# Performance work log

Hardware: AMD Instinct MI355X
Metric: run time of the kernel (lower is better)

Reference implementation:

```python
import jax, jax.numpy as jnp
import numpy as np

N, E, D_IN, HID, D_OUT, HEADS = 4096, 262144, 256, 256, 128, 4


def gcn_conv(x, edge_index, edge_weight, W, b):
    # PyG GCNConv: linear -> gcn_norm (add self loops, sym norm) -> scatter-add -> +bias
    n = x.shape[0]
    row, col = edge_index[0], edge_index[1]
    loop = jnp.arange(n)
    row_f = jnp.concatenate([row, loop])
    col_f = jnp.concatenate([col, loop])
    ew_f = jnp.concatenate([edge_weight, jnp.ones((n,), edge_weight.dtype)])
    deg = jax.ops.segment_sum(ew_f, col_f, num_segments=n)
    dinv = jnp.where(deg > 0, jax.lax.rsqrt(deg), 0.0)
    norm = dinv[row_f] * ew_f * dinv[col_f]  # [E+N]
    h = x @ W                                # [N, out]
    out = jax.ops.segment_sum(norm[:, None] * h[row_f], col_f, num_segments=n)
    return out + b


def mha(x, in_proj_w, in_proj_b, out_proj_w, out_proj_b):
    # torch.nn.MultiheadAttention, unbatched input [L, Emb], q=k=v=x
    L, Emb = x.shape
    dh = Emb // HEADS
    qkv = x @ in_proj_w.T + in_proj_b
    q, k, v = jnp.split(qkv, 3, axis=-1)
    rs = lambda t: t.reshape(L, HEADS, dh).transpose(1, 0, 2)  # [H, L, dh]
    q, k, v = rs(q), rs(k), rs(v)
    scores = jnp.einsum('hld,hmd->hlm', q, k) / np.float32(np.sqrt(dh))
    attn = jax.nn.softmax(scores, axis=-1)
    o = jnp.einsum('hlm,hmd->hld', attn, v).transpose(1, 0, 2).reshape(L, Emb)
    return o @ out_proj_w.T + out_proj_b


def setup_inputs() -> dict:
    key = jax.random.key(0)
    ks = jax.random.split(key, 12)
    s = 0.02
    return {
        'node_features': jax.random.normal(ks[0], (N, D_IN), jnp.float32),
        'edge_index': jax.random.randint(ks[1], (2, E), 0, N),
        'edge_weight': jax.random.uniform(ks[2], (E,), jnp.float32),
        'W1': jax.random.normal(ks[3], (D_IN, HID), jnp.float32) * s,
        'b1': jnp.zeros((HID,), jnp.float32),
        'W2': jax.random.normal(ks[4], (HID, HID), jnp.float32) * s,
        'b2': jnp.zeros((HID,), jnp.float32),
        'W3': jax.random.normal(ks[5], (HID, D_OUT), jnp.float32) * s,
        'b3': jnp.zeros((D_OUT,), jnp.float32),
        'in_proj_w': jax.random.normal(ks[6], (3 * HID, HID), jnp.float32) * s,
        'in_proj_b': jnp.zeros((3 * HID,), jnp.float32),
        'out_proj_w': jax.random.normal(ks[7], (HID, HID), jnp.float32) * s,
        'out_proj_b': jnp.zeros((HID,), jnp.float32),
    }


def reference(node_features, edge_index, edge_weight, W1, b1, W2, b2, W3, b3,
              in_proj_w, in_proj_b, out_proj_w, out_proj_b):
    ew = edge_weight.astype(jnp.float32)
    x = gcn_conv(node_features, edge_index, ew, W1, b1)
    x = jax.nn.relu(mha(x, in_proj_w, in_proj_b, out_proj_w, out_proj_b))
    # dropout is identity at inference
    x = gcn_conv(x, edge_index, ew, W2, b2)
    x = jax.nn.relu(mha(x, in_proj_w, in_proj_b, out_proj_w, out_proj_b))
    x = gcn_conv(x, edge_index, ew, W3, b3)
    return jax.nn.sigmoid(x)
```

## Files before the change

kernel.cpp:

```cpp
#include <hip/hip_runtime.h>
#include <math.h>

#define N_NODES 4096
#define N_EDGES 262144

typedef __attribute__((ext_vector_type(4))) float f32x4;
typedef __attribute__((ext_vector_type(8))) short s16x8;
typedef __attribute__((ext_vector_type(4))) unsigned short u16x4;

__device__ inline unsigned short f2bf(float f) {
    unsigned u = __builtin_bit_cast(unsigned, f);
    u += 0x7FFF + ((u >> 16) & 1);
    return (unsigned short)(u >> 16);
}
__device__ inline unsigned short f2bf_t(float f) {
    return (unsigned short)(__builtin_bit_cast(unsigned, f) >> 16);
}
__device__ inline float bf2f(unsigned short u) {
    unsigned x = ((unsigned)u) << 16;
    return __builtin_bit_cast(float, x);
}

#define SWZ(row, colb) (((row) << 7) + ((colb) ^ (((row) & 7) << 4)))

__global__ void prep_all(const float* __restrict__ x0, const float* __restrict__ ipw,
                         const float* __restrict__ opw, const float* __restrict__ ipb,
                         const float* __restrict__ W1, const float* __restrict__ W2,
                         const float* __restrict__ W3,
                         unsigned short* __restrict__ x0b, unsigned short* __restrict__ ipwb,
                         unsigned short* __restrict__ opwb, float* __restrict__ ipbs,
                         unsigned short* __restrict__ W1t, unsigned short* __restrict__ W2t,
                         unsigned short* __restrict__ W3t) {
    const int NA = 262144;
    const int NB = 49152;
    const int NC = 16384;
    const int ND1 = 65536, ND2 = 65536, ND3 = 32768;
    const int NE = 768;
    const int total = NA + NB + NC + ND1 + ND2 + ND3 + NE;
    for (int idx = blockIdx.x * blockDim.x + threadIdx.x; idx < total;
         idx += gridDim.x * blockDim.x) {
        int t = idx;
        if (t < NA) {
            int i = t * 4;
            f32x4 v = *(const f32x4*)(x0 + i);
            u16x4 o;
#pragma unroll
            for (int j = 0; j < 4; j++) o[j] = f2bf(v[j]);
            *(u16x4*)(x0b + i) = o;
            continue;
        }
        t -= NA;
        if (t < NB) {
            int i = t * 4;
            int r = i >> 8;
            float sc = (r >= 256 && r < 512) ? 0.1803369f : 1.0f;
            f32x4 v = *(const f32x4*)(ipw + i);
            u16x4 o;
#pragma unroll
            for (int j = 0; j < 4; j++) o[j] = f2bf(v[j] * sc);
            *(u16x4*)(ipwb + i) = o;
            continue;
        }
        t -= NB;
        if (t < NC) {
            int i = t * 4;
            f32x4 v = *(const f32x4*)(opw + i);
            u16x4 o;
#pragma unroll
            for (int j = 0; j < 4; j++) o[j] = f2bf(v[j]);
            *(u16x4*)(opwb + i) = o;
            continue;
        }
        t -= NC;
        if (t < ND1) {
            int r = t & 255, c = t >> 8;
            W1t[c * 256 + r] = f2bf(W1[r * 256 + c]);
            continue;
        }
        t -= ND1;
        if (t < ND2) {
            int r = t & 255, c = t >> 8;
            W2t[c * 256 + r] = f2bf(W2[r * 256 + c]);
            continue;
        }
        t -= ND2;
        if (t < ND3) {
            int r = t & 255, c = t >> 8;
            W3t[c * 256 + r] = f2bf(W3[r * 128 + c]);
            continue;
        }
        t -= ND3;
        {
            float sc = (t >= 256 && t < 512) ? 0.1803369f : 1.0f;
            ipbs[t] = ipb[t] * sc;
        }
    }
}

__global__ void deg_accum(const int* __restrict__ col, const float* __restrict__ ew,
                          float* deg, int* cnt) {
    for (int e = blockIdx.x * blockDim.x + threadIdx.x; e < N_EDGES;
         e += gridDim.x * blockDim.x) {
        int c = col[e];
        atomicAdd(&deg[c], ew[e]);
        atomicAdd(&cnt[c], 1);
    }
}

__global__ __launch_bounds__(1024) void scan_offsets(const int* __restrict__ cnt,
                                                     float* __restrict__ deg,
                                                     int* off, int* fill) {
    __shared__ int s[1024];
    int tid = threadIdx.x;
#pragma unroll
    for (int q = 0; q < 4; q++) {
        int i = tid * 4 + q;
        deg[i] = rsqrtf(deg[i] + 1.0f);
    }
    int c0 = cnt[tid * 4 + 0], c1 = cnt[tid * 4 + 1];
    int c2 = cnt[tid * 4 + 2], c3 = cnt[tid * 4 + 3];
    int lsum = c0 + c1 + c2 + c3;
    s[tid] = lsum;
    __syncthreads();
    for (int d = 1; d < 1024; d <<= 1) {
        int v = (tid >= d) ? s[tid - d] : 0;
        __syncthreads();
        s[tid] += v;
        __syncthreads();
    }
    int incl = s[tid];
    int base = incl - lsum;
    int o0 = base, o1 = base + c0, o2 = base + c0 + c1, o3 = base + c0 + c1 + c2;
    off[tid * 4 + 0] = o0;  fill[tid * 4 + 0] = o0;
    off[tid * 4 + 1] = o1;  fill[tid * 4 + 1] = o1;
    off[tid * 4 + 2] = o2;  fill[tid * 4 + 2] = o2;
    off[tid * 4 + 3] = o3;  fill[tid * 4 + 3] = o3;
    if (tid == 1023) off[4096] = incl;
}

__global__ void scatter_edges(const int* __restrict__ row, const int* __restrict__ col,
                              const float* __restrict__ ew, const float* __restrict__ dinv,
                              int* fill, unsigned long long* __restrict__ ep) {
    for (int e = blockIdx.x * blockDim.x + threadIdx.x; e < N_EDGES;
         e += gridDim.x * blockDim.x) {
        int r = row[e], c = col[e];
        int p = atomicAdd(&fill[c], 1);
        float w = dinv[r] * ew[e] * dinv[c];
        unsigned long long v =
            ((unsigned long long)__builtin_bit_cast(unsigned, w) << 32) | (unsigned)r;
        ep[p] = v;
    }
}

template <bool BIAS, int ACT, bool QKV>
__global__ __launch_bounds__(64) void gemm_bf16(const unsigned short* __restrict__ A,
                                                const unsigned short* __restrict__ B,
                                                const float* __restrict__ bias,
                                                unsigned short* __restrict__ C,
                                                unsigned short* __restrict__ Vt, int P) {
    int lane = threadIdx.x & 63;
    int lx = lane & 15, g = lane >> 4;
    int brow = blockIdx.y * 32, bcol = blockIdx.x * 64;
    const unsigned short* Ap0 = A + (size_t)(brow + lx) * 256 + g * 8;
    const unsigned short* Ap1 = Ap0 + 16 * 256;
    const unsigned short* Bp = B + (size_t)(bcol + lx) * 256 + g * 8;
    f32x4 acc[2][4];
#pragma unroll
    for (int mi = 0; mi < 2; mi++)
#pragma unroll
        for (int nt = 0; nt < 4; nt++) acc[mi][nt] = f32x4{0.f, 0.f, 0.f, 0.f};
#pragma unroll
    for (int kc = 0; kc < 8; kc++) {
        s16x8 a0 = *(const s16x8*)(Ap0 + kc * 32);
        s16x8 a1 = *(const s16x8*)(Ap1 + kc * 32);
#pragma unroll
        for (int nt = 0; nt < 4; nt++) {
            s16x8 b = *(const s16x8*)(Bp + (size_t)nt * 16 * 256 + kc * 32);
            acc[0][nt] = __builtin_amdgcn_mfma_f32_16x16x32_bf16(a0, b, acc[0][nt], 0, 0, 0);
            acc[1][nt] = __builtin_amdgcn_mfma_f32_16x16x32_bf16(a1, b, acc[1][nt], 0, 0, 0);
        }
    }
    bool isV = QKV && (bcol >= 512);
    if (!isV) {
#pragma unroll
        for (int mi = 0; mi < 2; mi++)
#pragma unroll
            for (int nt = 0; nt < 4; nt++)
#pragma unroll
                for (int r = 0; r < 4; r++) {
                    int row = brow + mi * 16 + g * 4 + r, col = bcol + nt * 16 + lx;
                    float v = acc[mi][nt][r];
                    if (BIAS) v += bias[col];
                    if (ACT == 1) v = fmaxf(v, 0.f);
                    C[(size_t)row * P + col] = f2bf(v);
                }
    } else {
        int head = (bcol - 512) >> 6;
#pragma unroll
        for (int mi = 0; mi < 2; mi++)
#pragma unroll
            for (int nt = 0; nt < 4; nt++) {
                int col = bcol + nt * 16 + lx;
                u16x4 vv;
#pragma unroll
                for (int r = 0; r < 4; r++) {
                    float v = acc[mi][nt][r];
                    if (BIAS) v += bias[col];
                    vv[r] = f2bf(v);
                }
                *(u16x4*)(Vt + (size_t)(head * 64 + nt * 16 + lx) * 4096 +
                          brow + mi * 16 + g * 4) = vv;
            }
    }
}

template <int P, bool SIG>
__global__ __launch_bounds__(64) void gcn_agg(const unsigned short* __restrict__ H,
                                              const int* __restrict__ off,
                                              const unsigned long long* __restrict__ ep,
                                              const float* __restrict__ dinv,
                                              const float* __restrict__ bias,
                                              unsigned short* __restrict__ outb,
                                              float* __restrict__ outf) {
    constexpr int CPT = P / 64;
    __shared__ unsigned long long se[64];
    int i = blockIdx.x, tid = threadIdx.x;
    float di = dinv[i];
    float d2 = di * di;
    float acc[CPT];
    if (CPT == 4) {
        u16x4 h = *(const u16x4*)(H + (size_t)i * P + tid * 4);
#pragma unroll
        for (int j = 0; j < 4; j++) acc[j] = d2 * bf2f(h[j]);
    } else {
        unsigned h = *(const unsigned*)(H + (size_t)i * P + tid * 2);
        acc[0] = d2 * bf2f((unsigned short)(h & 0xFFFF));
        acc[1] = d2 * bf2f((unsigned short)(h >> 16));
    }
    int beg = off[i], end = off[i + 1];
    for (int base = beg; base < end; base += 64) {
        int n = min(64, end - base);
        __syncthreads();
        if (tid < n) se[tid] = ep[base + tid];
        __syncthreads();
#pragma unroll 4
        for (int j = 0; j < n; j++) {
            unsigned long long v = se[j];
            int r = (int)(unsigned)v;
            float w = __builtin_bit_cast(float, (unsigned)(v >> 32));
            size_t rb = (size_t)r * P;
            if (CPT == 4) {
                u16x4 h = *(const u16x4*)(H + rb + tid * 4);
#pragma unroll
                for (int q = 0; q < 4; q++) acc[q] += w * bf2f(h[q]);
            } else {
                unsigned h = *(const unsigned*)(H + rb + tid * 2);
                acc[0] += w * bf2f((unsigned short)(h & 0xFFFF));
                acc[1] += w * bf2f((unsigned short)(h >> 16));
            }
        }
    }
#pragma unroll
    for (int j = 0; j < CPT; j++) {
        int c = tid * CPT + j;
        float v = acc[j] + bias[c];
        if (SIG) {
            v = 1.f / (1.f + exp2f(-v * 1.442695f));
            outf[(size_t)i * P + c] = v;
        } else {
            outb[(size_t)i * P + c] = f2bf(v);
        }
    }
}

__global__ __launch_bounds__(256) void attn_mfma(const unsigned short* __restrict__ qkv,
                                                 const unsigned short* __restrict__ Vt,
                                                 unsigned short* __restrict__ Po,
                                                 float* __restrict__ Pl) {
    __shared__ unsigned short Ks[2][64 * 64];
    __shared__ unsigned short Vs[2][64 * 64];
    __shared__ unsigned short Ps[4][16 * 64];

    int tid = threadIdx.x;
    int wid = tid >> 6, lane = tid & 63, g = lane >> 4, lx = lane & 15;
    int head = blockIdx.y, chunk = blockIdx.z;
    int qw = blockIdx.x * 64 + wid * 16;

    s16x8 qa[2];
#pragma unroll
    for (int kc = 0; kc < 2; kc++)
        qa[kc] = *(const s16x8*)(qkv + (size_t)(qw + lx) * 768 + head * 64 + kc * 32 + g * 8);

    int kr0 = tid >> 3, dc0 = tid & 7;
    int kr1 = kr0 + 32;
    int kt_beg = chunk * 16, kt_end = kt_beg + 16;

    const unsigned short* kp0 =
        qkv + 256 + head * 64 + (size_t)(kt_beg * 64 + kr0) * 768 + dc0 * 8;
    const unsigned short* kp1 = kp0 + (size_t)32 * 768;
    const unsigned short* vp0 =
        Vt + (size_t)head * 64 * 4096 + (size_t)kr0 * 4096 + kt_beg * 64 + dc0 * 8;
    const unsigned short* vp1 = vp0 + (size_t)32 * 4096;

    s16x8 stK[2], stV[2];
    auto issue = [&]() {
        stK[0] = *(const s16x8*)kp0;
        stK[1] = *(const s16x8*)kp1;
        stV[0] = *(const s16x8*)vp0;
        stV[1] = *(const s16x8*)vp1;
        kp0 += 64 * 768; kp1 += 64 * 768;
        vp0 += 64; vp1 += 64;
    };
    auto commit = [&](int b) {
        *(s16x8*)((char*)Ks[b] + SWZ(kr0, dc0 * 16)) = stK[0];
        *(s16x8*)((char*)Ks[b] + SWZ(kr1, dc0 * 16)) = stK[1];
        *(s16x8*)((char*)Vs[b] + SWZ(kr0, dc0 * 16)) = stV[0];
        *(s16x8*)((char*)Vs[b] + SWZ(kr1, dc0 * 16)) = stV[1];
    };

    float lreg[4] = {0.f, 0.f, 0.f, 0.f};
    f32x4 o[4];
#pragma unroll
    for (int dt = 0; dt < 4; dt++) o[dt] = f32x4{0.f, 0.f, 0.f, 0.f};

    char* PsW = (char*)Ps[wid];

    issue();
    commit(0);
    __syncthreads();

    for (int kt = kt_beg; kt < kt_end; kt++) {
        int cur = (kt - kt_beg) & 1;
        if (kt + 1 < kt_end) issue();

        f32x4 s4[4];
        __builtin_amdgcn_s_setprio(1);
#pragma unroll
        for (int nt = 0; nt < 4; nt++) {
            f32x4 acc = f32x4{0.f, 0.f, 0.f, 0.f};
#pragma unroll
            for (int kc = 0; kc < 2; kc++) {
                s16x8 kb = *(const s16x8*)((char*)Ks[cur] + SWZ(nt * 16 + lx, kc * 64 + g * 16));
                acc = __builtin_amdgcn_mfma_f32_16x16x32_bf16(qa[kc], kb, acc, 0, 0, 0);
            }
            s4[nt] = acc;
        }
        __builtin_amdgcn_s_setprio(0);

#pragma unroll
        for (int nt = 0; nt < 4; nt++)
#pragma unroll
            for (int r = 0; r < 4; r++) {
                float p = exp2f(fminf(s4[nt][r], 60.f));
                lreg[r] += p;
                *(unsigned short*)(PsW + SWZ(4 * g + r, (nt * 16 + lx) * 2)) = f2bf_t(p);
            }

        __builtin_amdgcn_s_setprio(1);
#pragma unroll
        for (int kc = 0; kc < 2; kc++) {
            s16x8 pa = *(const s16x8*)(PsW + SWZ(lx, kc * 64 + g * 16));
#pragma unroll
            for (int dt = 0; dt < 4; dt++) {
                s16x8 vb = *(const s16x8*)((char*)Vs[cur] + SWZ(dt * 16 + lx, kc * 64 + g * 16));
                o[dt] = __builtin_amdgcn_mfma_f32_16x16x32_bf16(pa, vb, o[dt], 0, 0, 0);
            }
        }
        __builtin_amdgcn_s_setprio(0);

        if (kt + 1 < kt_end) commit(1 - cur);
        __syncthreads();
    }

#pragma unroll
    for (int r = 0; r < 4; r++) {
        float ls = lreg[r];
        ls += __shfl_xor(ls, 1, 16);
        ls += __shfl_xor(ls, 2, 16);
        ls += __shfl_xor(ls, 4, 16);
        ls += __shfl_xor(ls, 8, 16);
        int qrow = qw + 4 * g + r;
        size_t base = (size_t)(chunk * 4 + head) * 4096 + qrow;
        if (lx == 0) Pl[base] = ls;
#pragma unroll
        for (int dt = 0; dt < 4; dt++)
            Po[base * 64 + dt * 16 + lx] = f2bf(o[dt][r]);
    }
}

__global__ __launch_bounds__(256) void attn_combine(const unsigned short* __restrict__ Po,
                                                    const float* __restrict__ Pl,
                                                    unsigned short* __restrict__ att) {
    int tid = threadIdx.x;
    int q = blockIdx.x * 4 + (tid >> 6);
    int lane = tid & 63;
    int head = lane >> 4, quad = lane & 15;
    float L = 0.f;
    f32x4 ov = {0.f, 0.f, 0.f, 0.f};
#pragma unroll
    for (int c = 0; c < 4; c++) {
        size_t base = (size_t)(c * 4 + head) * 4096 + q;
        L += Pl[base];
        u16x4 p = *(const u16x4*)(Po + base * 64 + quad * 4);
#pragma unroll
        for (int k = 0; k < 4; k++) ov[k] += bf2f(p[k]);
    }
    float inv = 1.0f / L;
    u16x4 r;
#pragma unroll
    for (int k = 0; k < 4; k++) r[k] = f2bf(ov[k] * inv);
    *(u16x4*)(att + (size_t)q * 256 + head * 64 + quad * 4) = r;
}

extern "C" void kernel_launch(void* const* d_in, const int* in_sizes, int n_in,
                              void* d_out, int out_size, void* d_ws, size_t ws_size,
                              hipStream_t stream) {
    const float* x0  = (const float*)d_in[0];
    const int*   eix = (const int*)d_in[1];
    const float* ew  = (const float*)d_in[2];
    const float* W1  = (const float*)d_in[3];
    const float* b1  = (const float*)d_in[4];
    const float* W2  = (const float*)d_in[5];
    const float* b2  = (const float*)d_in[6];
    const float* W3  = (const float*)d_in[7];
    const float* b3  = (const float*)d_in[8];
    const float* ipw = (const float*)d_in[9];
    const float* ipb = (const float*)d_in[10];
    const float* opw = (const float*)d_in[11];
    const float* opb = (const float*)d_in[12];
    float* out = (float*)d_out;

    char* ws = (char*)d_ws;
    size_t o = 0;
    auto alloc = [&](size_t bytes) -> void* {
        void* p = ws + o;
        o = (o + bytes + 255) & ~size_t(255);
        return p;
    };
    float* dinv  = (float*)alloc(N_NODES * 4);
    int*   cnt   = (int*)alloc(N_NODES * 4);
    int*   off   = (int*)alloc((N_NODES + 1) * 4);
    int*   fill  = (int*)alloc(N_NODES * 4);
    unsigned long long* ep = (unsigned long long*)alloc((size_t)N_EDGES * 8);
    unsigned short* x0b  = (unsigned short*)alloc((size_t)N_NODES * 256 * 2);
    unsigned short* W1t  = (unsigned short*)alloc(256 * 256 * 2);
    unsigned short* W2t  = (unsigned short*)alloc(256 * 256 * 2);
    unsigned short* W3t  = (unsigned short*)alloc(128 * 256 * 2);
    unsigned short* ipwb = (unsigned short*)alloc(768 * 256 * 2);
    unsigned short* opwb = (unsigned short*)alloc(256 * 256 * 2);
    float* ipbs          = (float*)alloc(768 * 4);
    unsigned short* Hb   = (unsigned short*)alloc((size_t)N_NODES * 256 * 2);
    unsigned short* XAb  = (unsigned short*)alloc((size_t)N_NODES * 256 * 2);
    unsigned short* XBb  = (unsigned short*)alloc((size_t)N_NODES * 256 * 2);
    unsigned short* QKVb = (unsigned short*)alloc((size_t)N_NODES * 768 * 2);
    unsigned short* Vt   = (unsigned short*)alloc((size_t)4 * 64 * 4096 * 2);
    unsigned short* Po   = (unsigned short*)alloc((size_t)16 * 4096 * 64 * 2);
    float* Pl            = (float*)alloc((size_t)16 * 4096 * 4);

    const int* row = eix;
    const int* col = eix + N_EDGES;

    hipMemsetAsync(dinv, 0, N_NODES * 4, stream);
    hipMemsetAsync(cnt, 0, N_NODES * 4, stream);
    prep_all<<<512, 256, 0, stream>>>(x0, ipw, opw, ipb, W1, W2, W3,
                                      x0b, ipwb, opwb, ipbs, W1t, W2t, W3t);
    deg_accum<<<512, 256, 0, stream>>>(col, ew, dinv, cnt);
    scan_offsets<<<1, 1024, 0, stream>>>(cnt, dinv, off, fill);
    scatter_edges<<<512, 256, 0, stream>>>(row, col, ew, dinv, fill, ep);

    gemm_bf16<false, 0, false><<<dim3(4, 128), 64, 0, stream>>>(x0b, W1t, nullptr, Hb, nullptr, 256);
    gcn_agg<256, false><<<N_NODES, 64, 0, stream>>>(Hb, off, ep, dinv, b1, XAb, nullptr);
    gemm_bf16<true, 0, true><<<dim3(12, 128), 64, 0, stream>>>(XAb, ipwb, ipbs, QKVb, Vt, 768);
    attn_mfma<<<dim3(64, 4, 4), 256, 0, stream>>>(QKVb, Vt, Po, Pl);
    attn_combine<<<N_NODES / 4, 256, 0, stream>>>(Po, Pl, Hb);
    gemm_bf16<true, 1, false><<<dim3(4, 128), 64, 0, stream>>>(Hb, opwb, opb, XBb, nullptr, 256);
    gemm_bf16<false, 0, false><<<dim3(4, 128), 64, 0, stream>>>(XBb, W2t, nullptr, Hb, nullptr, 256);
    gcn_agg<256, false><<<N_NODES, 64, 0, stream>>>(Hb, off, ep, dinv, b2, XAb, nullptr);
    gemm_bf16<true, 0, true><<<dim3(12, 128), 64, 0, stream>>>(XAb, ipwb, ipbs, QKVb, Vt, 768);
    attn_mfma<<<dim3(64, 4, 4), 256, 0, stream>>>(QKVb, Vt, Po, Pl);
    attn_combine<<<N_NODES / 4, 256, 0, stream>>>(Po, Pl, Hb);
    gemm_bf16<true, 1, false><<<dim3(4, 128), 64, 0, stream>>>(Hb, opwb, opb, XBb, nullptr, 256);
    gemm_bf16<false, 0, false><<<dim3(2, 128), 64, 0, stream>>>(XBb, W3t, nullptr, Hb, nullptr, 128);
    gcn_agg<128, true><<<N_NODES, 64, 0, stream>>>(Hb, off, ep, dinv, b3, nullptr, out);
}
```

Before: 303.8 us.

## Enlarge GEMM and attention per-wave tiles, batch edge staging in aggregation

The bf16 GEMM now computes a 64x64 tile per wave instead of 32x64, reusing each B fragment across four A fragments, and its grid is halved. The attention kernel processes 32 query rows per wave, computing S^T by swapping MFMA operands so P can be written as packed 8-byte stores, and its grid is halved. GCN aggregation stages 128 edges per shared-memory batch to halve barrier count. These changes aim to raise MFMA operand reuse and reduce LDS and barrier overhead, at the cost of higher register pressure and fewer blocks per launch (GEMM grids drop to 256-768 single-wave blocks).

```diff
diff --git a/kernel.cpp b/kernel.cpp
--- a/kernel.cpp
+++ b/kernel.cpp
@@ -7,6 +7,7 @@
 typedef __attribute__((ext_vector_type(4))) float f32x4;
 typedef __attribute__((ext_vector_type(8))) short s16x8;
 typedef __attribute__((ext_vector_type(4))) unsigned short u16x4;
+typedef __attribute__((ext_vector_type(2))) unsigned u32x2;
 
 __device__ inline unsigned short f2bf(float f) {
     unsigned u = __builtin_bit_cast(unsigned, f);
@@ -160,30 +161,34 @@
                                                 unsigned short* __restrict__ Vt, int P) {
     int lane = threadIdx.x & 63;
     int lx = lane & 15, g = lane >> 4;
-    int brow = blockIdx.y * 32, bcol = blockIdx.x * 64;
-    const unsigned short* Ap0 = A + (size_t)(brow + lx) * 256 + g * 8;
-    const unsigned short* Ap1 = Ap0 + 16 * 256;
+    int brow = blockIdx.y * 64, bcol = blockIdx.x * 64;
+    const unsigned short* Ap = A + (size_t)(brow + lx) * 256 + g * 8;
     const unsigned short* Bp = B + (size_t)(bcol + lx) * 256 + g * 8;
-    f32x4 acc[2][4];
-#pragma unroll
-    for (int mi = 0; mi < 2; mi++)
+    f32x4 acc[4][4];
+#pragma unroll
+    for (int mi = 0; mi < 4; mi++)
 #pragma unroll
         for (int nt = 0; nt < 4; nt++) acc[mi][nt] = f32x4{0.f, 0.f, 0.f, 0.f};
 #pragma unroll
     for (int kc = 0; kc < 8; kc++) {
-        s16x8 a0 = *(const s16x8*)(Ap0 + kc * 32);
-        s16x8 a1 = *(const s16x8*)(Ap1 + kc * 32);
-#pragma unroll
-        for (int nt = 0; nt < 4; nt++) {
-            s16x8 b = *(const s16x8*)(Bp + (size_t)nt * 16 * 256 + kc * 32);
-            acc[0][nt] = __builtin_amdgcn_mfma_f32_16x16x32_bf16(a0, b, acc[0][nt], 0, 0, 0);
-            acc[1][nt] = __builtin_amdgcn_mfma_f32_16x16x32_bf16(a1, b, acc[1][nt], 0, 0, 0);
-        }
+        s16x8 a[4], b[4];
+#pragma unroll
+        for (int mi = 0; mi < 4; mi++)
+            a[mi] = *(const s16x8*)(Ap + (size_t)mi * 16 * 256 + kc * 32);
+#pragma unroll
+        for (int nt = 0; nt < 4; nt++)
+            b[nt] = *(const s16x8*)(Bp + (size_t)nt * 16 * 256 + kc * 32);
+#pragma unroll
+        for (int mi = 0; mi < 4; mi++)
+#pragma unroll
+            for (int nt = 0; nt < 4; nt++)
+                acc[mi][nt] = __builtin_amdgcn_mfma_f32_16x16x32_bf16(a[mi], b[nt],
+                                                                      acc[mi][nt], 0, 0, 0);
     }
     bool isV = QKV && (bcol >= 512);
     if (!isV) {
 #pragma unroll
-        for (int mi = 0; mi < 2; mi++)
+        for (int mi = 0; mi < 4; mi++)
 #pragma unroll
             for (int nt = 0; nt < 4; nt++)
 #pragma unroll
@@ -197,7 +202,7 @@
     } else {
         int head = (bcol - 512) >> 6;
 #pragma unroll
-        for (int mi = 0; mi < 2; mi++)
+        for (int mi = 0; mi < 4; mi++)
 #pragma unroll
             for (int nt = 0; nt < 4; nt++) {
                 int col = bcol + nt * 16 + lx;
@@ -223,7 +228,7 @@
                                               unsigned short* __restrict__ outb,
                                               float* __restrict__ outf) {
     constexpr int CPT = P / 64;
-    __shared__ unsigned long long se[64];
+    __shared__ unsigned long long se[128];
     int i = blockIdx.x, tid = threadIdx.x;
     float di = dinv[i];
     float d2 = di * di;
@@ -238,10 +243,11 @@
         acc[1] = d2 * bf2f((unsigned short)(h >> 16));
     }
     int beg = off[i], end = off[i + 1];
-    for (int base = beg; base < end; base += 64) {
-        int n = min(64, end - base);
+    for (int base = beg; base < end; base += 128) {
+        int n = min(128, end - base);
         __syncthreads();
         if (tid < n) se[tid] = ep[base + tid];
+        if (tid + 64 < n) se[tid + 64] = ep[base + tid + 64];
         __syncthreads();
 #pragma unroll 4
         for (int j = 0; j < n; j++) {
@@ -279,17 +285,20 @@
                                                  float* __restrict__ Pl) {
     __shared__ unsigned short Ks[2][64 * 64];
     __shared__ unsigned short Vs[2][64 * 64];
-    __shared__ unsigned short Ps[4][16 * 64];
+    __shared__ unsigned short Ps[4][32 * 64];
 
     int tid = threadIdx.x;
     int wid = tid >> 6, lane = tid & 63, g = lane >> 4, lx = lane & 15;
     int head = blockIdx.y, chunk = blockIdx.z;
-    int qw = blockIdx.x * 64 + wid * 16;
-
-    s16x8 qa[2];
-#pragma unroll
-    for (int kc = 0; kc < 2; kc++)
-        qa[kc] = *(const s16x8*)(qkv + (size_t)(qw + lx) * 768 + head * 64 + kc * 32 + g * 8);
+    int qw = blockIdx.x * 128 + wid * 32;
+
+    s16x8 qa[2][2];
+#pragma unroll
+    for (int h = 0; h < 2; h++)
+#pragma unroll
+        for (int kc = 0; kc < 2; kc++)
+            qa[h][kc] = *(const s16x8*)(qkv + (size_t)(qw + h * 16 + lx) * 768 +
+                                        head * 64 + kc * 32 + g * 8);
 
     int kr0 = tid >> 3, dc0 = tid & 7;
     int kr1 = kr0 + 32;
@@ -318,10 +327,12 @@
         *(s16x8*)((char*)Vs[b] + SWZ(kr1, dc0 * 16)) = stV[1];
     };
 
-    float lreg[4] = {0.f, 0.f, 0.f, 0.f};
-    f32x4 o[4];
-#pragma unroll
-    for (int dt = 0; dt < 4; dt++) o[dt] = f32x4{0.f, 0.f, 0.f, 0.f};
+    float lreg[2] = {0.f, 0.f};
+    f32x4 o[2][4];
+#pragma unroll
+    for (int h = 0; h < 2; h++)
+#pragma unroll
+        for (int dt = 0; dt < 4; dt++) o[h][dt] = f32x4{0.f, 0.f, 0.f, 0.f};
 
     char* PsW = (char*)Ps[wid];
 
@@ -333,37 +344,48 @@
         int cur = (kt - kt_beg) & 1;
         if (kt + 1 < kt_end) issue();
 
-        f32x4 s4[4];
+        f32x4 s4[2][4];
         __builtin_amdgcn_s_setprio(1);
 #pragma unroll
         for (int nt = 0; nt < 4; nt++) {
-            f32x4 acc = f32x4{0.f, 0.f, 0.f, 0.f};
+            f32x4 a0 = f32x4{0.f, 0.f, 0.f, 0.f};
+            f32x4 a1 = f32x4{0.f, 0.f, 0.f, 0.f};
 #pragma unroll
             for (int kc = 0; kc < 2; kc++) {
                 s16x8 kb = *(const s16x8*)((char*)Ks[cur] + SWZ(nt * 16 + lx, kc * 64 + g * 16));
-                acc = __builtin_amdgcn_mfma_f32_16x16x32_bf16(qa[kc], kb, acc, 0, 0, 0);
+                a0 = __builtin_amdgcn_mfma_f32_16x16x32_bf16(kb, qa[0][kc], a0, 0, 0, 0);
+                a1 = __builtin_amdgcn_mfma_f32_16x16x32_bf16(kb, qa[1][kc], a1, 0, 0, 0);
             }
-            s4[nt] = acc;
+            s4[0][nt] = a0;
+            s4[1][nt] = a1;
         }
         __builtin_amdgcn_s_setprio(0);
 
 #pragma unroll
-        for (int nt = 0; nt < 4; nt++)
-#pragma unroll
-            for (int r = 0; r < 4; r++) {
-                float p = exp2f(fminf(s4[nt][r], 60.f));
-                lreg[r] += p;
-                *(unsigned short*)(PsW + SWZ(4 * g + r, (nt * 16 + lx) * 2)) = f2bf_t(p);
+        for (int h = 0; h < 2; h++)
+#pragma unroll
+            for (int nt = 0; nt < 4; nt++) {
+                float p0 = exp2f(fminf(s4[h][nt][0], 60.f));
+                float p1 = exp2f(fminf(s4[h][nt][1], 60.f));
+                float p2 = exp2f(fminf(s4[h][nt][2], 60.f));
+                float p3 = exp2f(fminf(s4[h][nt][3], 60.f));
+                lreg[h] += (p0 + p1) + (p2 + p3);
+                u32x2 w;
+                w[0] = (unsigned)f2bf_t(p0) | ((unsigned)f2bf_t(p1) << 16);
+                w[1] = (unsigned)f2bf_t(p2) | ((unsigned)f2bf_t(p3) << 16);
+                *(u32x2*)(PsW + SWZ(h * 16 + lx, nt * 32 + g * 8)) = w;
             }
 
         __builtin_amdgcn_s_setprio(1);
 #pragma unroll
         for (int kc = 0; kc < 2; kc++) {
-            s16x8 pa = *(const s16x8*)(PsW + SWZ(lx, kc * 64 + g * 16));
+            s16x8 pa0 = *(const s16x8*)(PsW + SWZ(lx, kc * 64 + g * 16));
+            s16x8 pa1 = *(const s16x8*)(PsW + SWZ(16 + lx, kc * 64 + g * 16));
 #pragma unroll
             for (int dt = 0; dt < 4; dt++) {
                 s16x8 vb = *(const s16x8*)((char*)Vs[cur] + SWZ(dt * 16 + lx, kc * 64 + g * 16));
-                o[dt] = __builtin_amdgcn_mfma_f32_16x16x32_bf16(pa, vb, o[dt], 0, 0, 0);
+                o[0][dt] = __builtin_amdgcn_mfma_f32_16x16x32_bf16(pa0, vb, o[0][dt], 0, 0, 0);
+                o[1][dt] = __builtin_amdgcn_mfma_f32_16x16x32_bf16(pa1, vb, o[1][dt], 0, 0, 0);
             }
         }
         __builtin_amdgcn_s_setprio(0);
@@ -373,18 +395,22 @@
     }
 
 #pragma unroll
-    for (int r = 0; r < 4; r++) {
-        float ls = lreg[r];
-        ls += __shfl_xor(ls, 1, 16);
-        ls += __shfl_xor(ls, 2, 16);
-        ls += __shfl_xor(ls, 4, 16);
-        ls += __shfl_xor(ls, 8, 16);
-        int qrow = qw + 4 * g + r;
-        size_t base = (size_t)(chunk * 4 + head) * 4096 + qrow;
-        if (lx == 0) Pl[base] = ls;
-#pragma unroll
-        for (int dt = 0; dt < 4; dt++)
-            Po[base * 64 + dt * 16 + lx] = f2bf(o[dt][r]);
+    for (int h = 0; h < 2; h++) {
+        float ls = lreg[h];
+        ls += __shfl_xor(ls, 16);
+        ls += __shfl_xor(ls, 32);
+        if (g == 0) {
+            int qrow = qw + h * 16 + lx;
+            Pl[(size_t)(chunk * 4 + head) * 4096 + qrow] = ls;
+        }
+#pragma unroll
+        for (int r = 0; r < 4; r++) {
+            int qrow = qw + h * 16 + 4 * g + r;
+            size_t base = (size_t)(chunk * 4 + head) * 4096 + qrow;
+#pragma unroll
+            for (int dt = 0; dt < 4; dt++)
+                Po[base * 64 + dt * 16 + lx] = f2bf(o[h][dt][r]);
+        }
     }
 }
 
@@ -468,18 +494,18 @@
     scan_offsets<<<1, 1024, 0, stream>>>(cnt, dinv, off, fill);
     scatter_edges<<<512, 256, 0, stream>>>(row, col, ew, dinv, fill, ep);
 
-    gemm_bf16<false, 0, false><<<dim3(4, 128), 64, 0, stream>>>(x0b, W1t, nullptr, Hb, nullptr, 256);
+    gemm_bf16<false, 0, false><<<dim3(4, 64), 64, 0, stream>>>(x0b, W1t, nullptr, Hb, nullptr, 256);
     gcn_agg<256, false><<<N_NODES, 64, 0, stream>>>(Hb, off, ep, dinv, b1, XAb, nullptr);
-    gemm_bf16<true, 0, true><<<dim3(12, 128), 64, 0, stream>>>(XAb, ipwb, ipbs, QKVb, Vt, 768);
-    attn_mfma<<<dim3(64, 4, 4), 256, 0, stream>>>(QKVb, Vt, Po, Pl);
+    gemm_bf16<true, 0, true><<<dim3(12, 64), 64, 0, stream>>>(XAb, ipwb, ipbs, QKVb, Vt, 768);
+    attn_mfma<<<dim3(32, 4, 4), 256, 0, stream>>>(QKVb, Vt, Po, Pl);
     attn_combine<<<N_NODES / 4, 256, 0, stream>>>(Po, Pl, Hb);
-    gemm_bf16<true, 1, false><<<dim3(4, 128), 64, 0, stream>>>(Hb, opwb, opb, XBb, nullptr, 256);
-    gemm_bf16<false, 0, false><<<dim3(4, 128), 64, 0, stream>>>(XBb, W2t, nullptr, Hb, nullptr, 256);
+    gemm_bf16<true, 1, false><<<dim3(4, 64), 64, 0, stream>>>(Hb, opwb, opb, XBb, nullptr, 256);
+    gemm_bf16<false, 0, false><<<dim3(4, 64), 64, 0, stream>>>(XBb, W2t, nullptr, Hb, nullptr, 256);
     gcn_agg<256, false><<<N_NODES, 64, 0, stream>>>(Hb, off, ep, dinv, b2, XAb, nullptr);
-    gemm_bf16<true, 0, true><<<dim3(12, 128), 64, 0, stream>>>(XAb, ipwb, ipbs, QKVb, Vt, 768);
-    attn_mfma<<<dim3(64, 4, 4), 256, 0, stream>>>(QKVb, Vt, Po, Pl);
+    gemm_bf16<true, 0, true><<<dim3(12, 64), 64, 0, stream>>>(XAb, ipwb, ipbs, QKVb, Vt, 768);
+    attn_mfma<<<dim3(32, 4, 4), 256, 0, stream>>>(QKVb, Vt, Po, Pl);
     attn_combine<<<N_NODES / 4, 256, 0, stream>>>(Po, Pl, Hb);
-    gemm_bf16<true, 1, false><<<dim3(4, 128), 64, 0, stream>>>(Hb, opwb, opb, XBb, nullptr, 256);
-    gemm_bf16<false, 0, false><<<dim3(2, 128), 64, 0, stream>>>(XBb, W3t, nullptr, Hb, nullptr, 128);
+    gemm_bf16<true, 1, false><<<dim3(4, 64), 64, 0, stream>>>(Hb, opwb, opb, XBb, nullptr, 256);
+    gemm_bf16<false, 0, false><<<dim3(2, 64), 64, 0, stream>>>(XBb, W3t, nullptr, Hb, nullptr, 128);
     gcn_agg<128, true><<<N_NODES, 64, 0, stream>>>(Hb, off, ep, dinv, b3, nullptr, out);
 }
```

Result: slower. 310.2 us (+2.1%).

## Deepen attention prefetch, remap blocks per XCD, batch more edges in aggregation

Applied to the files above, without the earlier changes.

The attention kernel now keeps two register stages of K/V in flight, so the global loads for a tile are issued two iterations ahead. The loop is unrolled by two so the LDS buffer indices become constants. The grid is flattened to 1D, and block IDs are remapped so that all blocks sharing one head/chunk's K/V land on the same XCD, which should improve L2 reuse. GCN aggregation stages 128 edges per shared-memory batch instead of 64, halving barrier rounds, at the cost of more registers and some risk of lower occupancy.

```diff
diff --git a/kernel.cpp b/kernel.cpp
--- a/kernel.cpp
+++ b/kernel.cpp
@@ -223,7 +223,7 @@
                                               unsigned short* __restrict__ outb,
                                               float* __restrict__ outf) {
     constexpr int CPT = P / 64;
-    __shared__ unsigned long long se[64];
+    __shared__ unsigned long long se[128];
     int i = blockIdx.x, tid = threadIdx.x;
     float di = dinv[i];
     float d2 = di * di;
@@ -238,10 +238,11 @@
         acc[1] = d2 * bf2f((unsigned short)(h >> 16));
     }
     int beg = off[i], end = off[i + 1];
-    for (int base = beg; base < end; base += 64) {
-        int n = min(64, end - base);
+    for (int base = beg; base < end; base += 128) {
+        int n = min(128, end - base);
         __syncthreads();
         if (tid < n) se[tid] = ep[base + tid];
+        if (tid + 64 < n) se[tid + 64] = ep[base + tid + 64];
         __syncthreads();
 #pragma unroll 4
         for (int j = 0; j < n; j++) {
@@ -273,6 +274,8 @@
     }
 }
 
+struct Stage { s16x8 K0, K1, V0, V1; };
+
 __global__ __launch_bounds__(256) void attn_mfma(const unsigned short* __restrict__ qkv,
                                                  const unsigned short* __restrict__ Vt,
                                                  unsigned short* __restrict__ Po,
@@ -283,8 +286,12 @@
 
     int tid = threadIdx.x;
     int wid = tid >> 6, lane = tid & 63, g = lane >> 4, lx = lane & 15;
-    int head = blockIdx.y, chunk = blockIdx.z;
-    int qw = blockIdx.x * 64 + wid * 16;
+    int bid = blockIdx.x;
+    int xcd = bid & 7, loc = bid >> 3;
+    int pair = xcd * 2 + (loc >> 6);
+    int qt = loc & 63;
+    int head = pair >> 2, chunk = pair & 3;
+    int qw = qt * 64 + wid * 16;
 
     s16x8 qa[2];
 #pragma unroll
@@ -293,7 +300,7 @@
 
     int kr0 = tid >> 3, dc0 = tid & 7;
     int kr1 = kr0 + 32;
-    int kt_beg = chunk * 16, kt_end = kt_beg + 16;
+    int kt_beg = chunk * 16;
 
     const unsigned short* kp0 =
         qkv + 256 + head * 64 + (size_t)(kt_beg * 64 + kr0) * 768 + dc0 * 8;
@@ -302,20 +309,20 @@
         Vt + (size_t)head * 64 * 4096 + (size_t)kr0 * 4096 + kt_beg * 64 + dc0 * 8;
     const unsigned short* vp1 = vp0 + (size_t)32 * 4096;
 
-    s16x8 stK[2], stV[2];
-    auto issue = [&]() {
-        stK[0] = *(const s16x8*)kp0;
-        stK[1] = *(const s16x8*)kp1;
-        stV[0] = *(const s16x8*)vp0;
-        stV[1] = *(const s16x8*)vp1;
-        kp0 += 64 * 768; kp1 += 64 * 768;
+    Stage sA, sB;
+    auto issue = [&](Stage& S) {
+        S.K0 = *(const s16x8*)kp0;
+        S.K1 = *(const s16x8*)kp1;
+        S.V0 = *(const s16x8*)vp0;
+        S.V1 = *(const s16x8*)vp1;
+        kp0 += (size_t)64 * 768; kp1 += (size_t)64 * 768;
         vp0 += 64; vp1 += 64;
     };
-    auto commit = [&](int b) {
-        *(s16x8*)((char*)Ks[b] + SWZ(kr0, dc0 * 16)) = stK[0];
-        *(s16x8*)((char*)Ks[b] + SWZ(kr1, dc0 * 16)) = stK[1];
-        *(s16x8*)((char*)Vs[b] + SWZ(kr0, dc0 * 16)) = stV[0];
-        *(s16x8*)((char*)Vs[b] + SWZ(kr1, dc0 * 16)) = stV[1];
+    auto commit = [&](const Stage& S, int b) {
+        *(s16x8*)((char*)Ks[b] + SWZ(kr0, dc0 * 16)) = S.K0;
+        *(s16x8*)((char*)Ks[b] + SWZ(kr1, dc0 * 16)) = S.K1;
+        *(s16x8*)((char*)Vs[b] + SWZ(kr0, dc0 * 16)) = S.V0;
+        *(s16x8*)((char*)Vs[b] + SWZ(kr1, dc0 * 16)) = S.V1;
     };
 
     float lreg[4] = {0.f, 0.f, 0.f, 0.f};
@@ -325,14 +332,7 @@
 
     char* PsW = (char*)Ps[wid];
 
-    issue();
-    commit(0);
-    __syncthreads();
-
-    for (int kt = kt_beg; kt < kt_end; kt++) {
-        int cur = (kt - kt_beg) & 1;
-        if (kt + 1 < kt_end) issue();
-
+    auto compute = [&](int cur) {
         f32x4 s4[4];
         __builtin_amdgcn_s_setprio(1);
 #pragma unroll
@@ -367,8 +367,21 @@
             }
         }
         __builtin_amdgcn_s_setprio(0);
-
-        if (kt + 1 < kt_end) commit(1 - cur);
+    };
+
+    issue(sA);
+    commit(sA, 0);
+    issue(sB);
+    __syncthreads();
+
+    for (int it = 0; it < 16; it += 2) {
+        if (it + 2 < 16) issue(sA);
+        compute(0);
+        commit(sB, 1);
+        __syncthreads();
+        if (it + 3 < 16) issue(sB);
+        compute(1);
+        if (it + 2 < 16) commit(sA, 0);
         __syncthreads();
     }
 
@@ -471,13 +484,13 @@
     gemm_bf16<false, 0, false><<<dim3(4, 128), 64, 0, stream>>>(x0b, W1t, nullptr, Hb, nullptr, 256);
     gcn_agg<256, false><<<N_NODES, 64, 0, stream>>>(Hb, off, ep, dinv, b1, XAb, nullptr);
     gemm_bf16<true, 0, true><<<dim3(12, 128), 64, 0, stream>>>(XAb, ipwb, ipbs, QKVb, Vt, 768);
-    attn_mfma<<<dim3(64, 4, 4), 256, 0, stream>>>(QKVb, Vt, Po, Pl);
+    attn_mfma<<<1024, 256, 0, stream>>>(QKVb, Vt, Po, Pl);
     attn_combine<<<N_NODES / 4, 256, 0, stream>>>(Po, Pl, Hb);
     gemm_bf16<true, 1, false><<<dim3(4, 128), 64, 0, stream>>>(Hb, opwb, opb, XBb, nullptr, 256);
     gemm_bf16<false, 0, false><<<dim3(4, 128), 64, 0, stream>>>(XBb, W2t, nullptr, Hb, nullptr, 256);
     gcn_agg<256, false><<<N_NODES, 64, 0, stream>>>(Hb, off, ep, dinv, b2, XAb, nullptr);
     gemm_bf16<true, 0, true><<<dim3(12, 128), 64, 0, stream>>>(XAb, ipwb, ipbs, QKVb, Vt, 768);
-    attn_mfma<<<dim3(64, 4, 4), 256, 0, stream>>>(QKVb, Vt, Po, Pl);
+    attn_mfma<<<1024, 256, 0, stream>>>(QKVb, Vt, Po, Pl);
     attn_combine<<<N_NODES / 4, 256, 0, stream>>>(Po, Pl, Hb);
     gemm_bf16<true, 1, false><<<dim3(4, 128), 64, 0, stream>>>(Hb, opwb, opb, XBb, nullptr, 256);
     gemm_bf16<false, 0, false><<<dim3(2, 128), 64, 0, stream>>>(XBb, W3t, nullptr, Hb, nullptr, 128);
```

Result: no change. 302.9 us (-0.3%).
